# Performance work log

Hardware: AMD Instinct MI355X
Metric: run time of the kernel (lower is better)

The kernel has to match this reference:

```python
import jax, jax.numpy as jnp
import numpy as np

K0 = 16
TAU = -2.053748910631823
EPS = 1e-06


def setup_inputs() -> dict:
    key = jax.random.key(0)
    k1, k2, k3 = jax.random.split(key, 3)
    B, DIN, DOUT = 32768, 1024, 1024
    x = jax.random.normal(k1, (B, DIN), dtype=jnp.float32)
    weight = jax.random.normal(k2, (DOUT, DIN), dtype=jnp.float32) * 0.02
    bias = jax.random.normal(k3, (DOUT,), dtype=jnp.float32) * 0.02
    return {"x": x, "weight": weight, "bias": bias}


def reference(x, weight, bias):
    # Kernel loads x and w as fp16 and accumulates in fp32.
    x16 = x.astype(jnp.float16)        # [B, DIN]
    w16 = weight.astype(jnp.float16)   # [DOUT, DIN]

    xa, wa = x16[:, :K0], w16[:, :K0]
    # Warmup partial dot product over the first K0 columns: y1[b,n] = sum_k x[b,k]*w[n,k]
    y1 = jnp.einsum("bk,nk->bn", xa, wa, preferred_element_type=jnp.float32)
    # s2[b,n] = sum_k (x[b,k]*w[n,k])^2 = sum_k x^2 * w^2
    s2 = jnp.einsum("bk,nk->bn", xa * xa, wa * wa, preferred_element_type=jnp.float32)

    denom = jnp.sqrt(s2 / (K0 + EPS) + EPS)
    tstat = jnp.abs(y1) / jnp.maximum(denom, EPS)
    passed = tstat < TAU                     # early-terminate mask (true => skip remaining cols)
    still_active = ~passed                   # [B, DOUT]

    # Remaining columns contribute only where still_active.
    rest = jnp.einsum("bk,nk->bn", x16[:, K0:], w16[:, K0:], preferred_element_type=jnp.float32)
    acc = y1 + rest * still_active.astype(jnp.float32)

    out = acc + bias.astype(jnp.float32)
    return out.astype(x.dtype)
```

## Files before the change

### kernel.cpp

```cpp
#include <hip/hip_runtime.h>

typedef _Float16 f16;
typedef f16 f16x2 __attribute__((ext_vector_type(2)));
typedef f16 f16x4 __attribute__((ext_vector_type(4)));
typedef f16 f16x8 __attribute__((ext_vector_type(8)));
typedef float f32x4 __attribute__((ext_vector_type(4)));

constexpr int Mdim = 32768, Ndim = 1024, Kdim = 1024;
constexpr int BM = 256, BN = 256, BK = 64;
constexpr int NT = Kdim / BK;

static __device__ inline f16x2 cvt2(float a, float b) {
    return __builtin_bit_cast(f16x2, __builtin_amdgcn_cvt_pkrtz(a, b));
}
static __device__ inline f16x4 cvt4(float4 v) {
    f16x2 lo = cvt2(v.x, v.y), hi = cvt2(v.z, v.w);
    return __builtin_shufflevector(lo, hi, 0, 1, 2, 3);
}
static __device__ inline void bar() {
    asm volatile("" ::: "memory");
    __builtin_amdgcn_s_barrier();
    asm volatile("" ::: "memory");
}

__global__ __launch_bounds__(512, 2)
void etrow_gemm(const float* __restrict__ X, const float* __restrict__ W,
                const float* __restrict__ bias, float* __restrict__ out)
{
    __shared__ f16 As[2][BM * BK];
    __shared__ f16 Bs[2][BN * BK];

    const int bid = blockIdx.x;
    const int cpx = gridDim.x >> 3;
    const int wg  = (bid & 7) * cpx + (bid >> 3);
    const int mIdx = wg >> 2;
    const int nIdx = wg & 3;

    const int tid  = threadIdx.x;
    const int lane = tid & 63;
    const int wave = tid >> 6;
    const int wr   = (wave >> 2) * 128;
    const int wc   = (wave & 3) * 64;

    const int r0 = tid >> 4;
    const int c4 = tid & 15;

    const float* Xb = X + (size_t)mIdx * BM * Kdim;
    const float* Wb = W + (size_t)nIdx * BN * Kdim;

    float4 S[8];
    f32x4 acc[8][4] = {};

    auto loadA = [&](int kt) {
        const float* p = Xb + kt * BK + c4 * 4;
        #pragma unroll
        for (int q = 0; q < 8; ++q)
            S[q] = *(const float4*)(p + (q * 32 + r0) * Kdim);
    };
    auto loadB = [&](int kt) {
        const float* p = Wb + kt * BK + c4 * 4;
        #pragma unroll
        for (int q = 0; q < 8; ++q)
            S[q] = *(const float4*)(p + (q * 32 + r0) * Kdim);
    };
    auto cvtWrite = [&](f16* lds) {
        #pragma unroll
        for (int q = 0; q < 8; ++q) {
            const int r = q * 32 + r0;
            const int byte = (r * 128 + c4 * 8) ^ ((r & 7) << 4);
            *(f16x4*)((char*)lds + byte) = cvt4(S[q]);
        }
    };

    auto computeSub = [&](const f16* Ab, const f16* Bb, int s) {
        f16x8 af[8], bf[4];
        const int kb = s * 64 + (lane >> 4) * 16;
        #pragma unroll
        for (int i = 0; i < 8; ++i) {
            const int r = wr + i * 16 + (lane & 15);
            const int byte = (r * 128 + kb) ^ ((r & 7) << 4);
            af[i] = *(const f16x8*)((const char*)Ab + byte);
        }
        #pragma unroll
        for (int j = 0; j < 4; ++j) {
            const int r = wc + j * 16 + (lane & 15);
            const int byte = (r * 128 + kb) ^ ((r & 7) << 4);
            bf[j] = *(const f16x8*)((const char*)Bb + byte);
        }
        #pragma unroll
        for (int i = 0; i < 8; ++i)
            #pragma unroll
            for (int j = 0; j < 4; ++j)
                acc[i][j] = __builtin_amdgcn_mfma_f32_16x16x32_f16(
                    af[i], bf[j], acc[i][j], 0, 0, 0);
    };

    loadA(0); cvtWrite(&As[0][0]);
    loadB(0); cvtWrite(&Bs[0][0]);
    loadA(1);
    asm volatile("s_waitcnt lgkmcnt(0)" ::: "memory");
    bar();

    for (int t = 0; t < NT; ++t) {
        const int cur = t & 1, nxt = cur ^ 1;
        if (t + 1 < NT) { cvtWrite(&As[nxt][0]); loadB(t + 1); }
        computeSub(&As[cur][0], &Bs[cur][0], 0);
        if (t + 1 < NT) { cvtWrite(&Bs[nxt][0]); }
        if (t + 2 < NT) { loadA(t + 2); }
        computeSub(&As[cur][0], &Bs[cur][0], 1);
        asm volatile("s_waitcnt lgkmcnt(0)" ::: "memory");
        bar();
    }

    const int col0  = nIdx * BN + wc + (lane & 15);
    const int rbase = mIdx * BM + wr + (lane >> 4) * 4;
    float bv[4];
    #pragma unroll
    for (int n = 0; n < 4; ++n) bv[n] = bias[col0 + n * 16];

    #pragma unroll
    for (int m = 0; m < 8; ++m) {
        #pragma unroll
        for (int j = 0; j < 4; ++j) {
            const int row = rbase + m * 16 + j;
            float* o = out + (size_t)row * Ndim + col0;
            #pragma unroll
            for (int n = 0; n < 4; ++n)
                o[n * 16] = acc[m][n][j] + bv[n];
        }
    }
}

extern "C" void kernel_launch(void* const* d_in, const int* in_sizes, int n_in,
                              void* d_out, int out_size, void* d_ws, size_t ws_size,
                              hipStream_t stream) {
    const float* X  = (const float*)d_in[0];
    const float* W  = (const float*)d_in[1];
    const float* bs = (const float*)d_in[2];
    float* out = (float*)d_out;
    const int grid = (Mdim / BM) * (Ndim / BN);
    etrow_gemm<<<grid, 512, 0, stream>>>(X, W, bs, out);
}
```

Before: 98.98 us.

## Restructure GEMM main loop into barrier-phased ping-pong with separate A/B staging registers

```diff
diff --git a/kernel.cpp b/kernel.cpp
--- a/kernel.cpp
+++ b/kernel.cpp
@@ -22,6 +22,9 @@
     __builtin_amdgcn_s_barrier();
     asm volatile("" ::: "memory");
 }
+static __device__ inline void lgkm0() {
+    asm volatile("s_waitcnt lgkmcnt(0)" ::: "memory");
+}
 
 __global__ __launch_bounds__(512, 2)
 void etrow_gemm(const float* __restrict__ X, const float* __restrict__ W,
@@ -45,71 +48,90 @@
     const int r0 = tid >> 4;
     const int c4 = tid & 15;
 
-    const float* Xb = X + (size_t)mIdx * BM * Kdim;
-    const float* Wb = W + (size_t)nIdx * BN * Kdim;
+    const float* xthr = X + (size_t)mIdx * BM * Kdim + r0 * Kdim + c4 * 4;
+    const float* wthr = W + (size_t)nIdx * BN * Kdim + r0 * Kdim + c4 * 4;
+    const int wbyte = (r0 * 128 + c4 * 8) ^ ((r0 & 7) << 4);
+    const int abyte = ((wr + (lane & 15)) * 128 + (lane >> 4) * 16) ^ ((lane & 7) << 4);
+    const int bbyte = ((wc + (lane & 15)) * 128 + (lane >> 4) * 16) ^ ((lane & 7) << 4);
+    char* const Ab = (char*)&As[0][0];
+    char* const Bb = (char*)&Bs[0][0];
 
-    float4 S[8];
+    float4 SA[8], SB[8];
     f32x4 acc[8][4] = {};
 
-    auto loadA = [&](int kt) {
-        const float* p = Xb + kt * BK + c4 * 4;
+    auto issueA = [&](int kt) {
+        const float* p = xthr + kt * BK;
         #pragma unroll
         for (int q = 0; q < 8; ++q)
-            S[q] = *(const float4*)(p + (q * 32 + r0) * Kdim);
+            SA[q] = *(const float4*)(p + q * 32 * Kdim);
     };
-    auto loadB = [&](int kt) {
-        const float* p = Wb + kt * BK + c4 * 4;
+    auto issueB = [&](int kt) {
+        const float* p = wthr + kt * BK;
         #pragma unroll
         for (int q = 0; q < 8; ++q)
-            S[q] = *(const float4*)(p + (q * 32 + r0) * Kdim);
+            SB[q] = *(const float4*)(p + q * 32 * Kdim);
     };
-    auto cvtWrite = [&](f16* lds) {
+    auto cvtWrA = [&](int bufoff) {
         #pragma unroll
-        for (int q = 0; q < 8; ++q) {
-            const int r = q * 32 + r0;
-            const int byte = (r * 128 + c4 * 8) ^ ((r & 7) << 4);
-            *(f16x4*)((char*)lds + byte) = cvt4(S[q]);
-        }
+        for (int q = 0; q < 8; ++q)
+            *(f16x4*)(Ab + bufoff + wbyte + q * 4096) = cvt4(SA[q]);
+    };
+    auto cvtWrB = [&](int bufoff) {
+        #pragma unroll
+        for (int q = 0; q < 8; ++q)
+            *(f16x4*)(Bb + bufoff + wbyte + q * 4096) = cvt4(SB[q]);
     };
 
-    auto computeSub = [&](const f16* Ab, const f16* Bb, int s) {
-        f16x8 af[8], bf[4];
-        const int kb = s * 64 + (lane >> 4) * 16;
+    auto phase = [&](int co, int p) {
+        f16x8 af[4], bf[4];
         #pragma unroll
-        for (int i = 0; i < 8; ++i) {
-            const int r = wr + i * 16 + (lane & 15);
-            const int byte = (r * 128 + kb) ^ ((r & 7) << 4);
-            af[i] = *(const f16x8*)((const char*)Ab + byte);
-        }
+        for (int mi = 0; mi < 4; ++mi)
+            af[mi] = *(const f16x8*)(Ab + co + ((abyte + (p * 4 + mi) * 2048)));
         #pragma unroll
-        for (int j = 0; j < 4; ++j) {
-            const int r = wc + j * 16 + (lane & 15);
-            const int byte = (r * 128 + kb) ^ ((r & 7) << 4);
-            bf[j] = *(const f16x8*)((const char*)Bb + byte);
-        }
+        for (int j = 0; j < 4; ++j)
+            bf[j] = *(const f16x8*)(Bb + co + ((bbyte + j * 2048)));
+        bar();
+        lgkm0();
+        __builtin_amdgcn_s_setprio(1);
         #pragma unroll
-        for (int i = 0; i < 8; ++i)
+        for (int mi = 0; mi < 4; ++mi)
             #pragma unroll
             for (int j = 0; j < 4; ++j)
-                acc[i][j] = __builtin_amdgcn_mfma_f32_16x16x32_f16(
-                    af[i], bf[j], acc[i][j], 0, 0, 0);
+                acc[p * 4 + mi][j] = __builtin_amdgcn_mfma_f32_16x16x32_f16(
+                    af[mi], bf[j], acc[p * 4 + mi][j], 0, 0, 0);
+        #pragma unroll
+        for (int mi = 0; mi < 4; ++mi)
+            af[mi] = *(const f16x8*)(Ab + co + ((abyte + (p * 4 + mi) * 2048) ^ 64));
+        #pragma unroll
+        for (int j = 0; j < 4; ++j)
+            bf[j] = *(const f16x8*)(Bb + co + ((bbyte + j * 2048) ^ 64));
+        #pragma unroll
+        for (int mi = 0; mi < 4; ++mi)
+            #pragma unroll
+            for (int j = 0; j < 4; ++j)
+                acc[p * 4 + mi][j] = __builtin_amdgcn_mfma_f32_16x16x32_f16(
+                    af[mi], bf[j], acc[p * 4 + mi][j], 0, 0, 0);
+        __builtin_amdgcn_s_setprio(0);
+        bar();
     };
 
-    loadA(0); cvtWrite(&As[0][0]);
-    loadB(0); cvtWrite(&Bs[0][0]);
-    loadA(1);
-    asm volatile("s_waitcnt lgkmcnt(0)" ::: "memory");
+    issueA(0); cvtWrA(0);
+    issueB(0); cvtWrB(0);
+    issueA(1); issueB(1);
+    lgkm0();
     bar();
 
     for (int t = 0; t < NT; ++t) {
-        const int cur = t & 1, nxt = cur ^ 1;
-        if (t + 1 < NT) { cvtWrite(&As[nxt][0]); loadB(t + 1); }
-        computeSub(&As[cur][0], &Bs[cur][0], 0);
-        if (t + 1 < NT) { cvtWrite(&Bs[nxt][0]); }
-        if (t + 2 < NT) { loadA(t + 2); }
-        computeSub(&As[cur][0], &Bs[cur][0], 1);
-        asm volatile("s_waitcnt lgkmcnt(0)" ::: "memory");
-        bar();
+        const int co = (t & 1) << 15;
+        const int no = co ^ 32768;
+        const bool h1 = t + 1 < NT, h2 = t + 2 < NT;
+
+        if (h1) cvtWrA(no);
+        if (h2) issueA(t + 2);
+        phase(co, 0);
+        if (h1) cvtWrB(no);
+        if (h2) issueB(t + 2);
+        phase(co, 1);
     }
 
     const int col0  = nIdx * BN + wc + (lane & 15);
```

Result: slower. 109.0 us (+10.1%).
